# Kernel optimization log

Measured on AMD Instinct MI355X. Metric: run time of the kernel, lower is better.

## Reference

```python
import jax, jax.numpy as jnp
import numpy as np

B, C, H, W = 2, 128, 64, 64  # in_channels == mlp_dim == 128 (residual requires equality)
MLP = 128


def setup_inputs() -> dict:
    key = jax.random.key(0)
    ks = jax.random.split(key, 12)
    s = 1.0 / np.sqrt(C)
    inp = {
        "x": jax.random.normal(ks[0], (B, C, H, W), jnp.float32),
        "y": jax.random.normal(ks[1], (B, C, H, W), jnp.float32),
        # stacked params for the 4 TransLayers: [4, out, in] weights, [4, out] biases
        "Wq": jax.random.uniform(ks[2], (4, MLP, C), jnp.float32, -s, s),
        "bq": jax.random.uniform(ks[3], (4, MLP), jnp.float32, -s, s),
        "Wk": jax.random.uniform(ks[4], (4, MLP, C), jnp.float32, -s, s),
        "bk": jax.random.uniform(ks[5], (4, MLP), jnp.float32, -s, s),
        "Wv": jax.random.uniform(ks[6], (4, MLP, C), jnp.float32, -s, s),
        "bv": jax.random.uniform(ks[7], (4, MLP), jnp.float32, -s, s),
        "Wo": jax.random.uniform(ks[8], (4, MLP, C), jnp.float32, -s, s),
        "bo": jax.random.uniform(ks[9], (4, MLP), jnp.float32, -s, s),
    }
    return inp


def _conv1x1_relu(x, w, b):
    # x: [B,C,H,W], w: [O,C], b: [O]  -> [B,O,H,W]
    return jax.nn.relu(jnp.einsum('bchw,oc->bohw', x, w) + b[None, :, None, None])


def _trans_layer(x, y, wq, bq, wk, bk, wv, bv, wo, bo):
    Q = _conv1x1_relu(x, wq, bq)  # [B,C,H,W]
    K = _conv1x1_relu(y, wk, bk)
    V = _conv1x1_relu(y, wv, bv)
    b, c, h, w = Q.shape
    n = h * w
    Qf = Q.reshape(b, c, n).transpose(0, 2, 1)  # [B,N,C]
    Kf = K.reshape(b, c, n)                      # [B,C,N]
    Vf = V.reshape(b, c, n).transpose(0, 2, 1)   # [B,N,C]
    attn = jax.nn.softmax(jnp.einsum('bnc,bcm->bnm', Qf, Kf), axis=-1)  # unscaled, [B,N,N]
    wV = jnp.einsum('bnm,bmc->bnc', attn, Vf)    # [B,N,C]
    wV = wV.transpose(0, 2, 1).reshape(b, c, h, w)
    return _conv1x1_relu(wV, wo, bo) + x


def reference(x, y, Wq, bq, Wk, bk, Wv, bv, Wo, bo):
    layer = lambda i, a, b_: _trans_layer(a, b_, Wq[i], bq[i], Wk[i], bk[i],
                                          Wv[i], bv[i], Wo[i], bo[i])
    fuse_xy = layer(0, x, y)
    fuse_yz = layer(1, y, x)
    fuse_xx = layer(2, fuse_xy, fuse_xy)
    fuse_yy = layer(3, fuse_yz, fuse_yz)
    return fuse_xx + fuse_yy
```

## Files before the change

kernel.cpp:

```cpp
#include <hip/hip_runtime.h>
#include <math.h>

#define C 128
#define NSP 4096
#define LOG2E 1.4426950408889634f

typedef __attribute__((ext_vector_type(8))) short short8;
typedef __attribute__((ext_vector_type(4))) float f32x4;
typedef __attribute__((ext_vector_type(16))) float f32x16;

static __device__ __forceinline__ unsigned short f2bf(float f) {
    union { float f; unsigned u; } a; a.f = f;
    unsigned r = a.u + 0x7fffu + ((a.u >> 16) & 1u);
    return (unsigned short)(r >> 16);
}

static __device__ __forceinline__ float bf2f(unsigned short s) {
    union { unsigned u; float f; } a; a.u = (unsigned)s << 16;
    return a.f;
}

static __device__ __forceinline__ unsigned pkbf(float a, float b) {
    union { float f; unsigned u; } ua, ub; ua.f = a; ub.f = b;
    return __builtin_amdgcn_perm(ub.u + 0x8000u, ua.u + 0x8000u, 0x07060302u);
}

static __device__ __forceinline__ float ex2(float x) {
#if __has_builtin(__builtin_amdgcn_exp2f)
    return __builtin_amdgcn_exp2f(x);
#else
    return exp2f(x);
#endif
}

static __device__ __forceinline__ f32x4 mfma16(short8 a, short8 b, f32x4 c) {
    return __builtin_amdgcn_mfma_f32_16x16x32_bf16(a, b, c, 0, 0, 0);
}

static __device__ __forceinline__ f32x16 mfma32(short8 a, short8 b, f32x16 c) {
    return __builtin_amdgcn_mfma_f32_32x32x16_bf16(a, b, c, 0, 0, 0);
}

__global__ __launch_bounds__(256)
void prep_kernel(const float* __restrict__ Wq, const float* __restrict__ Wk,
                 const float* __restrict__ Wv, const float* __restrict__ Wo,
                 unsigned short* __restrict__ Wb)
{
    int gid = blockIdx.x * 256 + threadIdx.x;
    int base = gid * 8;
    int mat = base >> 14;
    int off = base & 16383;
    const float* src = (mat < 4)  ? (Wq + (size_t)mat * 16384)
                     : (mat < 8)  ? (Wk + (size_t)(mat - 4) * 16384)
                     : (mat < 12) ? (Wv + (size_t)(mat - 8) * 16384)
                                  : (Wo + (size_t)(mat - 12) * 16384);
    float scale = (mat < 4) ? LOG2E : 1.0f;
    float4 v0 = *reinterpret_cast<const float4*>(src + off);
    float4 v1 = *reinterpret_cast<const float4*>(src + off + 4);
    uint4 u;
    u.x = pkbf(v0.x * scale, v0.y * scale);
    u.y = pkbf(v0.z * scale, v0.w * scale);
    u.z = pkbf(v1.x * scale, v1.y * scale);
    u.w = pkbf(v1.z * scale, v1.w * scale);
    *reinterpret_cast<uint4*>(Wb + base) = u;
}

static __device__ __forceinline__ void stage_wb(const unsigned short* __restrict__ Wm,
                                                unsigned short* __restrict__ Wl, int t) {
#pragma unroll
    for (int i = 0; i < 8; i++) {
        int idx = i * 256 + t;
        int o = idx >> 4, c8 = (idx & 15) << 3;
        *reinterpret_cast<uint4*>(&Wl[o * 136 + c8]) =
            *reinterpret_cast<const uint4*>(Wm + o * C + c8);
    }
}

static __device__ __forceinline__ void stage_in(const float* __restrict__ In, int n0,
                                                unsigned short* __restrict__ Il, int t) {
#pragma unroll
    for (int i = 0; i < 8; i++) {
        int idx = i * 256 + t;
        int c = idx >> 4, n4 = (idx & 15) << 2;
        float4 v = *reinterpret_cast<const float4*>(In + (size_t)c * NSP + n0 + n4);
        Il[(n4 + 0) * 136 + c] = f2bf(v.x);
        Il[(n4 + 1) * 136 + c] = f2bf(v.y);
        Il[(n4 + 2) * 136 + c] = f2bf(v.z);
        Il[(n4 + 3) * 136 + c] = f2bf(v.w);
    }
}

static __device__ __forceinline__ void stage_sum32(const unsigned short* __restrict__ Op,
                                                   const float* __restrict__ Lp,
                                                   int jb, int nks, int n0,
                                                   unsigned short* __restrict__ Il, int t) {
#pragma unroll
    for (int i = 0; i < 2; i++) {
        int idx = i * 256 + t;
        int n = idx >> 4, c8 = (idx & 15) << 3;
        float o[8];
#pragma unroll
        for (int j = 0; j < 8; j++) o[j] = 0.0f;
        float Ls = 0.0f;
        for (int k = 0; k < nks; k++) {
            size_t kjb = (size_t)(k * 4 + jb);
            Ls += Lp[kjb * NSP + n0 + n];
            union { uint4 v; unsigned short s[8]; } u;
            u.v = *reinterpret_cast<const uint4*>(Op + (kjb * NSP + n0 + n) * C + c8);
#pragma unroll
            for (int j = 0; j < 8; j++) o[j] += bf2f(u.s[j]);
        }
        float inv = 1.0f / Ls;
        union { uint4 v; unsigned u[4]; } w;
        w.u[0] = pkbf(o[0] * inv, o[1] * inv);
        w.u[1] = pkbf(o[2] * inv, o[3] * inv);
        w.u[2] = pkbf(o[4] * inv, o[5] * inv);
        w.u[3] = pkbf(o[6] * inv, o[7] * inv);
        *reinterpret_cast<uint4*>(&Il[n * 136 + c8]) = w.v;
    }
}

__global__ __launch_bounds__(256)
void qkv_kernel(const float* __restrict__ qs0, const float* __restrict__ qs1,
                const float* __restrict__ kv0, const float* __restrict__ kv1,
                const unsigned short* __restrict__ Wb,
                const float* __restrict__ bq, const float* __restrict__ bk,
                const float* __restrict__ bv,
                int layer_base,
                unsigned short* __restrict__ Qb, unsigned short* __restrict__ Kb,
                unsigned short* __restrict__ Vb)
{
    __shared__ __align__(16) unsigned short Wl[128 * 136];
    __shared__ __align__(16) unsigned short Il[64 * 136];
    const int t = threadIdx.x;
    const int ntile = blockIdx.x, kind = blockIdx.y, jb = blockIdx.z;
    const int job = jb >> 1, b = jb & 1, layer = layer_base + job;
    const float* src = (kind == 0) ? (job ? qs1 : qs0) : (job ? kv1 : kv0);
    const float* In = src + (size_t)b * C * NSP;
    const unsigned short* Wm = Wb + (size_t)(kind * 4 + layer) * 16384;
    const float* bias = ((kind == 0) ? bq : (kind == 1) ? bk : bv) + layer * C;
    unsigned short* Out = ((kind == 0) ? Qb : (kind == 1) ? Kb : Vb) + (size_t)jb * NSP * C;
    const float scale = (kind == 0) ? LOG2E : 1.0f;
    const int n0 = ntile * 64;

    stage_wb(Wm, Wl, t);
    stage_in(In, n0, Il, t);
    __syncthreads();

    const int lane = t & 63, w = t >> 6, l15 = lane & 15, quad = lane >> 4;

    if (kind <= 1) {
        f32x4 acc[4][2];
#pragma unroll
        for (int nt = 0; nt < 4; nt++)
#pragma unroll
            for (int ot = 0; ot < 2; ot++)
#pragma unroll
                for (int r = 0; r < 4; r++) acc[nt][ot][r] = 0.0f;
#pragma unroll
        for (int ks = 0; ks < 4; ks++) {
            int co = ks * 32 + quad * 8;
            short8 b0 = *reinterpret_cast<const short8*>(&Wl[(w * 32 + l15) * 136 + co]);
            short8 b1 = *reinterpret_cast<const short8*>(&Wl[(w * 32 + 16 + l15) * 136 + co]);
#pragma unroll
            for (int nt = 0; nt < 4; nt++) {
                short8 a = *reinterpret_cast<const short8*>(&Il[(nt * 16 + l15) * 136 + co]);
                acc[nt][0] = mfma16(a, b0, acc[nt][0]);
                acc[nt][1] = mfma16(a, b1, acc[nt][1]);
            }
        }
        float bz0 = bias[w * 32 + l15] * scale;
        float bz1 = bias[w * 32 + 16 + l15] * scale;
#pragma unroll
        for (int nt = 0; nt < 4; nt++)
#pragma unroll
            for (int ot = 0; ot < 2; ot++)
#pragma unroll
                for (int r = 0; r < 4; r++) {
                    float v = fmaxf(acc[nt][ot][r] + (ot ? bz1 : bz0), 0.0f);
                    int n = n0 + nt * 16 + quad * 4 + r;
                    int o = w * 32 + ot * 16 + l15;
                    Out[(size_t)n * C + o] = f2bf(v);
                }
    } else {
        f32x4 acc[2][4];
#pragma unroll
        for (int ot = 0; ot < 2; ot++)
#pragma unroll
            for (int nt = 0; nt < 4; nt++)
#pragma unroll
                for (int r = 0; r < 4; r++) acc[ot][nt][r] = 0.0f;
#pragma unroll
        for (int ks = 0; ks < 4; ks++) {
            int co = ks * 32 + quad * 8;
            short8 a0 = *reinterpret_cast<const short8*>(&Wl[(w * 32 + l15) * 136 + co]);
            short8 a1 = *reinterpret_cast<const short8*>(&Wl[(w * 32 + 16 + l15) * 136 + co]);
#pragma unroll
            for (int nt = 0; nt < 4; nt++) {
                short8 bb = *reinterpret_cast<const short8*>(&Il[(nt * 16 + l15) * 136 + co]);
                acc[0][nt] = mfma16(a0, bb, acc[0][nt]);
                acc[1][nt] = mfma16(a1, bb, acc[1][nt]);
            }
        }
#pragma unroll
        for (int ot = 0; ot < 2; ot++)
#pragma unroll
            for (int r = 0; r < 4; r++) {
                int o = w * 32 + ot * 16 + quad * 4 + r;
                float bz = bias[o];
#pragma unroll
                for (int nt = 0; nt < 4; nt++) {
                    float v = fmaxf(acc[ot][nt][r] + bz, 0.0f);
                    Out[(size_t)o * NSP + n0 + nt * 16 + l15] = f2bf(v);
                }
            }
    }
}

__global__ __launch_bounds__(512)
void attn_kernel(const unsigned short* __restrict__ Qb, const unsigned short* __restrict__ Kb,
                 const unsigned short* __restrict__ Vb, unsigned short* __restrict__ Op,
                 float* __restrict__ Lp, int iters)
{
    __shared__ __align__(16) unsigned short Kl[2][32 * 136];
    __shared__ __align__(16) unsigned short Vl[2][128 * 40];
    const int t = threadIdx.x, lane = t & 63;
    const int l31 = lane & 31, hi = lane >> 5;

    const int ksz = gridDim.z;
    const int nwg = gridDim.x * gridDim.y * ksz;
    const int linear = blockIdx.x + gridDim.x * (blockIdx.y + gridDim.y * blockIdx.z);
    const int cpx = nwg >> 3;
    const int wid = (linear & 7) * cpx + (linear >> 3);
    const int ntile = wid & 15;
    const int r2 = wid >> 4;
    const int jb = r2 / ksz, kc = r2 % ksz;

    const int n0 = ntile * 256 + (t >> 6) * 32;
    const int m_begin = kc * iters * 32;
    const unsigned short* Q = Qb + (size_t)jb * NSP * C;
    const unsigned short* K = Kb + (size_t)jb * NSP * C;
    const unsigned short* V = Vb + (size_t)jb * NSP * C;

    short8 qf[8];
#pragma unroll
    for (int ks = 0; ks < 8; ks++)
        qf[ks] = *reinterpret_cast<const short8*>(
            Q + (size_t)(n0 + l31) * C + ks * 16 + hi * 8);

    f32x16 o_acc[4];
#pragma unroll
    for (int ct = 0; ct < 4; ct++)
#pragma unroll
        for (int r = 0; r < 16; r++) o_acc[ct][r] = 0.0f;
    float L = 0.0f;

    uint4 kreg, vreg;
    const int km_ = t >> 4, kc8_ = (t & 15) << 3;
    const int vc_ = t >> 2, vm8_ = (t & 3) << 3;

#define ATT_LOAD(BLK)                                                                  \
    {                                                                                  \
        int mb_ = m_begin + (BLK) * 32;                                                \
        kreg = *reinterpret_cast<const uint4*>(K + (size_t)(mb_ + km_) * C + kc8_);    \
        vreg = *reinterpret_cast<const uint4*>(V + (size_t)vc_ * NSP + mb_ + vm8_);    \
    }

#define ATT_STORE(BUF)                                                                 \
    {                                                                                  \
        *reinterpret_cast<uint4*>(&Kl[BUF][km_ * 136 + kc8_]) = kreg;                  \
        *reinterpret_cast<uint4*>(&Vl[BUF][vc_ * 40 + vm8_]) = vreg;                   \
    }

    ATT_LOAD(0);
    ATT_STORE(0);
    if (iters > 1) ATT_LOAD(1);
    __syncthreads();

    int cur = 0;
    for (int blk = 0; blk < iters; blk++) {
        const unsigned short* Kc = &Kl[cur][0];
        const unsigned short* Vc = &Vl[cur][0];

        f32x16 s;
#pragma unroll
        for (int r = 0; r < 16; r++) s[r] = 0.0f;
        __builtin_amdgcn_s_setprio(1);
#pragma unroll
        for (int ks = 0; ks < 8; ks++) {
            short8 ka = *reinterpret_cast<const short8*>(&Kc[l31 * 136 + ks * 16 + hi * 8]);
            s = mfma32(ka, qf[ks], s);
        }
        __builtin_amdgcn_s_setprio(0);

        if (blk + 1 < iters) {
            ATT_STORE(cur ^ 1);
            if (blk + 2 < iters) ATT_LOAD(blk + 2);
        }

        float ls = 0.0f;
#pragma unroll
        for (int r = 0; r < 16; r++) {
            s[r] = ex2(s[r]);
            ls += s[r];
        }
        L += ls;

        unsigned a0 = pkbf(s[0], s[1]),  a1 = pkbf(s[2], s[3]);
        unsigned b0 = pkbf(s[4], s[5]),  b1 = pkbf(s[6], s[7]);
        unsigned c0 = pkbf(s[8], s[9]),  c1 = pkbf(s[10], s[11]);
        unsigned d0 = pkbf(s[12], s[13]), d1 = pkbf(s[14], s[15]);
        asm("v_permlane32_swap_b32 %0, %1" : "+v"(a0), "+v"(b0));
        asm("v_permlane32_swap_b32 %0, %1" : "+v"(a1), "+v"(b1));
        asm("v_permlane32_swap_b32 %0, %1" : "+v"(c0), "+v"(d0));
        asm("v_permlane32_swap_b32 %0, %1" : "+v"(c1), "+v"(d1));
        union { uint4 u; short8 s8; } f0u, f1u;
        f0u.u = make_uint4(a0, a1, b0, b1);
        f1u.u = make_uint4(c0, c1, d0, d1);

        __builtin_amdgcn_s_setprio(1);
#pragma unroll
        for (int ct = 0; ct < 4; ct++) {
            short8 v0 = *reinterpret_cast<const short8*>(&Vc[(ct * 32 + l31) * 40 + hi * 8]);
            short8 v1 = *reinterpret_cast<const short8*>(&Vc[(ct * 32 + l31) * 40 + 16 + hi * 8]);
            o_acc[ct] = mfma32(v0, f0u.s8, o_acc[ct]);
            o_acc[ct] = mfma32(v1, f1u.s8, o_acc[ct]);
        }
        __builtin_amdgcn_s_setprio(0);

        __syncthreads();
        cur ^= 1;
    }

#undef ATT_LOAD
#undef ATT_STORE

    const size_t kjb = (size_t)(kc * 4 + jb);
    float Lv = L + __shfl_xor(L, 32);
    if (lane < 32) Lp[kjb * NSP + n0 + l31] = Lv;

    unsigned short* Ob = Op + kjb * NSP * C;
    const int n = n0 + l31;
    unsigned short* On = Ob + (size_t)n * C + hi * 4;
#pragma unroll
    for (int ct = 0; ct < 4; ct++)
#pragma unroll
        for (int rb = 0; rb < 4; rb++) {
            int r0 = rb * 4;
            uint2 u;
            u.x = pkbf(o_acc[ct][r0 + 0], o_acc[ct][r0 + 1]);
            u.y = pkbf(o_acc[ct][r0 + 2], o_acc[ct][r0 + 3]);
            *reinterpret_cast<uint2*>(On + ct * 32 + rb * 8) = u;
        }
}

__global__ __launch_bounds__(256)
void proj_kernel(const unsigned short* __restrict__ Op, const float* __restrict__ Lp, int nks,
                 const unsigned short* __restrict__ Wb,
                 const float* __restrict__ bo, int layer_base,
                 const float* __restrict__ res0, const float* __restrict__ res1,
                 float* __restrict__ out0, float* __restrict__ out1)
{
    __shared__ __align__(16) unsigned short Wl[128 * 136];
    __shared__ __align__(16) unsigned short Il[32 * 136];
    const int t = threadIdx.x;
    const int ntile = blockIdx.x, jb = blockIdx.y;
    const int job = jb >> 1, b = jb & 1, layer = layer_base + job;
    const float* bias = bo + layer * C;
    const float* res = (job ? res1 : res0) + (size_t)b * C * NSP;
    float* out = (job ? out1 : out0) + (size_t)b * C * NSP;
    const int n0 = ntile * 32;

    stage_wb(Wb + (size_t)(12 + layer) * 16384, Wl, t);
    stage_sum32(Op, Lp, jb, nks, n0, Il, t);
    __syncthreads();

    const int lane = t & 63, w = t >> 6, l15 = lane & 15, quad = lane >> 4;
    f32x4 acc[2][2];
#pragma unroll
    for (int ot = 0; ot < 2; ot++)
#pragma unroll
        for (int nt = 0; nt < 2; nt++)
#pragma unroll
            for (int r = 0; r < 4; r++) acc[ot][nt][r] = 0.0f;
#pragma unroll
    for (int ks = 0; ks < 4; ks++) {
        int co = ks * 32 + quad * 8;
        short8 a0 = *reinterpret_cast<const short8*>(&Wl[(w * 32 + l15) * 136 + co]);
        short8 a1 = *reinterpret_cast<const short8*>(&Wl[(w * 32 + 16 + l15) * 136 + co]);
#pragma unroll
        for (int nt = 0; nt < 2; nt++) {
            short8 bb = *reinterpret_cast<const short8*>(&Il[(nt * 16 + l15) * 136 + co]);
            acc[0][nt] = mfma16(a0, bb, acc[0][nt]);
            acc[1][nt] = mfma16(a1, bb, acc[1][nt]);
        }
    }
#pragma unroll
    for (int ot = 0; ot < 2; ot++)
#pragma unroll
        for (int r = 0; r < 4; r++) {
            int o = w * 32 + ot * 16 + quad * 4 + r;
            float bz = bias[o];
#pragma unroll
            for (int nt = 0; nt < 2; nt++) {
                int n = n0 + nt * 16 + l15;
                float v = fmaxf(acc[ot][nt][r] + bz, 0.0f) + res[(size_t)o * NSP + n];
                out[(size_t)o * NSP + n] = v;
            }
        }
}

__global__ __launch_bounds__(256)
void final_kernel(const unsigned short* __restrict__ Op, const float* __restrict__ Lp, int nks,
                  const unsigned short* __restrict__ Wb,
                  const float* __restrict__ bo,
                  const float* __restrict__ fuse0, const float* __restrict__ fuse1,
                  float* __restrict__ out)
{
    __shared__ __align__(16) unsigned short Wl[128 * 136];
    __shared__ __align__(16) unsigned short Il[32 * 136];
    const int t = threadIdx.x;
    const int ntile = blockIdx.x, b = blockIdx.y;
    const int n0 = ntile * 32;
    const int lane = t & 63, w = t >> 6, l15 = lane & 15, quad = lane >> 4;

    float tot[2][2][4];
#pragma unroll
    for (int ot = 0; ot < 2; ot++)
#pragma unroll
        for (int nt = 0; nt < 2; nt++)
#pragma unroll
            for (int r = 0; r < 4; r++) tot[ot][nt][r] = 0.0f;

    for (int j = 0; j < 2; j++) {
        if (j) __syncthreads();
        int layer = 2 + j;
        stage_wb(Wb + (size_t)(12 + layer) * 16384, Wl, t);
        stage_sum32(Op, Lp, j * 2 + b, nks, n0, Il, t);
        __syncthreads();

        f32x4 acc[2][2];
#pragma unroll
        for (int ot = 0; ot < 2; ot++)
#pragma unroll
            for (int nt = 0; nt < 2; nt++)
#pragma unroll
                for (int r = 0; r < 4; r++) acc[ot][nt][r] = 0.0f;
#pragma unroll
        for (int ks = 0; ks < 4; ks++) {
            int co = ks * 32 + quad * 8;
            short8 a0 = *reinterpret_cast<const short8*>(&Wl[(w * 32 + l15) * 136 + co]);
            short8 a1 = *reinterpret_cast<const short8*>(&Wl[(w * 32 + 16 + l15) * 136 + co]);
#pragma unroll
            for (int nt = 0; nt < 2; nt++) {
                short8 bb = *reinterpret_cast<const short8*>(&Il[(nt * 16 + l15) * 136 + co]);
                acc[0][nt] = mfma16(a0, bb, acc[0][nt]);
                acc[1][nt] = mfma16(a1, bb, acc[1][nt]);
            }
        }
        const float* bias = bo + layer * C;
        const float* fuse = (j ? fuse1 : fuse0) + (size_t)b * C * NSP;
#pragma unroll
        for (int ot = 0; ot < 2; ot++)
#pragma unroll
            for (int r = 0; r < 4; r++) {
                int o = w * 32 + ot * 16 + quad * 4 + r;
                float bz = bias[o];
#pragma unroll
                for (int nt = 0; nt < 2; nt++) {
                    int n = n0 + nt * 16 + l15;
                    tot[ot][nt][r] += fmaxf(acc[ot][nt][r] + bz, 0.0f) + fuse[(size_t)o * NSP + n];
                }
            }
    }
#pragma unroll
    for (int ot = 0; ot < 2; ot++)
#pragma unroll
        for (int r = 0; r < 4; r++) {
            int o = w * 32 + ot * 16 + quad * 4 + r;
#pragma unroll
            for (int nt = 0; nt < 2; nt++) {
                int n = n0 + nt * 16 + l15;
                out[(size_t)b * C * NSP + (size_t)o * NSP + n] = tot[ot][nt][r];
            }
        }
}

extern "C" void kernel_launch(void* const* d_in, const int* in_sizes, int n_in,
                              void* d_out, int out_size, void* d_ws, size_t ws_size,
                              hipStream_t stream)
{
    (void)in_sizes; (void)n_in; (void)out_size;
    const float* x  = (const float*)d_in[0];
    const float* y  = (const float*)d_in[1];
    const float* Wq = (const float*)d_in[2];
    const float* bq = (const float*)d_in[3];
    const float* Wk = (const float*)d_in[4];
    const float* bk = (const float*)d_in[5];
    const float* Wv = (const float*)d_in[6];
    const float* bv = (const float*)d_in[7];
    const float* Wo = (const float*)d_in[8];
    const float* bo = (const float*)d_in[9];
    float* out = (float*)d_out;
    char* ws = (char*)d_ws;

    int ks = (ws_size >= 38010880u) ? 4 : 2;
    int iters = 128 / ks;

    unsigned short* Qb = (unsigned short*)(ws);
    unsigned short* Kb = (unsigned short*)(ws + (4u << 20));
    unsigned short* Vb = (unsigned short*)(ws + (8u << 20));
    unsigned short* Op = (unsigned short*)(ws + (12u << 20));
    size_t op_bytes = (size_t)ks * 4 * NSP * C * 2;
    float* Lp = (float*)(ws + (12u << 20) + op_bytes);
    float* fuse0 = Lp + (size_t)ks * 4 * NSP;
    float* fuse1 = fuse0 + (size_t)2 * C * NSP;
    unsigned short* Wb = (unsigned short*)(fuse1 + (size_t)2 * C * NSP);

    prep_kernel<<<dim3(128), 256, 0, stream>>>(Wq, Wk, Wv, Wo, Wb);

    qkv_kernel<<<dim3(64, 3, 4), 256, 0, stream>>>(x, y, y, x, Wb, bq, bk, bv, 0,
                                                   Qb, Kb, Vb);
    attn_kernel<<<dim3(16, 4, ks), 512, 0, stream>>>(Qb, Kb, Vb, Op, Lp, iters);
    proj_kernel<<<dim3(128, 4), 256, 0, stream>>>(Op, Lp, ks, Wb, bo, 0, x, y, fuse0, fuse1);

    qkv_kernel<<<dim3(64, 3, 4), 256, 0, stream>>>(fuse0, fuse1, fuse0, fuse1, Wb,
                                                   bq, bk, bv, 2, Qb, Kb, Vb);
    attn_kernel<<<dim3(16, 4, ks), 512, 0, stream>>>(Qb, Kb, Vb, Op, Lp, iters);
    final_kernel<<<dim3(128, 2), 256, 0, stream>>>(Op, Lp, ks, Wb, bo, fuse0, fuse1, out);
}
```

Baseline: 186.4 us.

## Double attention K/V block size to halve barriers; coalesce input staging loads

```diff
diff --git a/kernel.cpp b/kernel.cpp
--- a/kernel.cpp
+++ b/kernel.cpp
@@ -79,14 +79,19 @@
 static __device__ __forceinline__ void stage_in(const float* __restrict__ In, int n0,
                                                 unsigned short* __restrict__ Il, int t) {
 #pragma unroll
-    for (int i = 0; i < 8; i++) {
+    for (int i = 0; i < 4; i++) {
         int idx = i * 256 + t;
-        int c = idx >> 4, n4 = (idx & 15) << 2;
-        float4 v = *reinterpret_cast<const float4*>(In + (size_t)c * NSP + n0 + n4);
-        Il[(n4 + 0) * 136 + c] = f2bf(v.x);
-        Il[(n4 + 1) * 136 + c] = f2bf(v.y);
-        Il[(n4 + 2) * 136 + c] = f2bf(v.z);
-        Il[(n4 + 3) * 136 + c] = f2bf(v.w);
+        int n = idx & 63, cb = idx >> 6;
+        float v[8];
+#pragma unroll
+        for (int j = 0; j < 8; j++)
+            v[j] = In[(size_t)(cb * 8 + j) * NSP + n0 + n];
+        uint4 u;
+        u.x = pkbf(v[0], v[1]);
+        u.y = pkbf(v[2], v[3]);
+        u.z = pkbf(v[4], v[5]);
+        u.w = pkbf(v[6], v[7]);
+        *reinterpret_cast<uint4*>(&Il[n * 136 + cb * 8]) = u;
     }
 }
 
@@ -222,8 +227,8 @@
                  const unsigned short* __restrict__ Vb, unsigned short* __restrict__ Op,
                  float* __restrict__ Lp, int iters)
 {
-    __shared__ __align__(16) unsigned short Kl[2][32 * 136];
-    __shared__ __align__(16) unsigned short Vl[2][128 * 40];
+    __shared__ __align__(16) unsigned short Kl[2][64 * 136];
+    __shared__ __align__(16) unsigned short Vl[2][128 * 72];
     const int t = threadIdx.x, lane = t & 63;
     const int l31 = lane & 31, hi = lane >> 5;
 
@@ -237,7 +242,7 @@
     const int jb = r2 / ksz, kc = r2 % ksz;
 
     const int n0 = ntile * 256 + (t >> 6) * 32;
-    const int m_begin = kc * iters * 32;
+    const int m_begin = kc * iters * 64;
     const unsigned short* Q = Qb + (size_t)jb * NSP * C;
     const unsigned short* K = Kb + (size_t)jb * NSP * C;
     const unsigned short* V = Vb + (size_t)jb * NSP * C;
@@ -255,21 +260,29 @@
         for (int r = 0; r < 16; r++) o_acc[ct][r] = 0.0f;
     float L = 0.0f;
 
-    uint4 kreg, vreg;
-    const int km_ = t >> 4, kc8_ = (t & 15) << 3;
-    const int vc_ = t >> 2, vm8_ = (t & 3) << 3;
-
-#define ATT_LOAD(BLK)                                                                  \
-    {                                                                                  \
-        int mb_ = m_begin + (BLK) * 32;                                                \
-        kreg = *reinterpret_cast<const uint4*>(K + (size_t)(mb_ + km_) * C + kc8_);    \
-        vreg = *reinterpret_cast<const uint4*>(V + (size_t)vc_ * NSP + mb_ + vm8_);    \
-    }
-
-#define ATT_STORE(BUF)                                                                 \
-    {                                                                                  \
-        *reinterpret_cast<uint4*>(&Kl[BUF][km_ * 136 + kc8_]) = kreg;                  \
-        *reinterpret_cast<uint4*>(&Vl[BUF][vc_ * 40 + vm8_]) = vreg;                   \
+    uint4 kreg[2], vreg[2];
+
+#define ATT_LOAD(BLK)                                                                     \
+    {                                                                                     \
+        int mb_ = m_begin + (BLK) * 64;                                                   \
+        _Pragma("unroll") for (int i = 0; i < 2; i++) {                                   \
+            int idx = i * 512 + t;                                                        \
+            int m_ = idx >> 4, c8_ = (idx & 15) << 3;                                     \
+            kreg[i] = *reinterpret_cast<const uint4*>(K + (size_t)(mb_ + m_) * C + c8_);  \
+            int c_ = idx >> 3, m8_ = (idx & 7) << 3;                                      \
+            vreg[i] = *reinterpret_cast<const uint4*>(V + (size_t)c_ * NSP + mb_ + m8_);  \
+        }                                                                                 \
+    }
+
+#define ATT_STORE(BUF)                                                                    \
+    {                                                                                     \
+        _Pragma("unroll") for (int i = 0; i < 2; i++) {                                   \
+            int idx = i * 512 + t;                                                        \
+            int m_ = idx >> 4, c8_ = (idx & 15) << 3;                                     \
+            *reinterpret_cast<uint4*>(&Kl[BUF][m_ * 136 + c8_]) = kreg[i];                \
+            int c_ = idx >> 3, m8_ = (idx & 7) << 3;                                      \
+            *reinterpret_cast<uint4*>(&Vl[BUF][c_ * 72 + m8_]) = vreg[i];                 \
+        }                                                                                 \
     }
 
     ATT_LOAD(0);
@@ -282,51 +295,57 @@
         const unsigned short* Kc = &Kl[cur][0];
         const unsigned short* Vc = &Vl[cur][0];
 
-        f32x16 s;
-#pragma unroll
-        for (int r = 0; r < 16; r++) s[r] = 0.0f;
-        __builtin_amdgcn_s_setprio(1);
-#pragma unroll
-        for (int ks = 0; ks < 8; ks++) {
-            short8 ka = *reinterpret_cast<const short8*>(&Kc[l31 * 136 + ks * 16 + hi * 8]);
-            s = mfma32(ka, qf[ks], s);
-        }
-        __builtin_amdgcn_s_setprio(0);
-
-        if (blk + 1 < iters) {
-            ATT_STORE(cur ^ 1);
-            if (blk + 2 < iters) ATT_LOAD(blk + 2);
-        }
-
-        float ls = 0.0f;
-#pragma unroll
-        for (int r = 0; r < 16; r++) {
-            s[r] = ex2(s[r]);
-            ls += s[r];
-        }
-        L += ls;
-
-        unsigned a0 = pkbf(s[0], s[1]),  a1 = pkbf(s[2], s[3]);
-        unsigned b0 = pkbf(s[4], s[5]),  b1 = pkbf(s[6], s[7]);
-        unsigned c0 = pkbf(s[8], s[9]),  c1 = pkbf(s[10], s[11]);
-        unsigned d0 = pkbf(s[12], s[13]), d1 = pkbf(s[14], s[15]);
-        asm("v_permlane32_swap_b32 %0, %1" : "+v"(a0), "+v"(b0));
-        asm("v_permlane32_swap_b32 %0, %1" : "+v"(a1), "+v"(b1));
-        asm("v_permlane32_swap_b32 %0, %1" : "+v"(c0), "+v"(d0));
-        asm("v_permlane32_swap_b32 %0, %1" : "+v"(c1), "+v"(d1));
-        union { uint4 u; short8 s8; } f0u, f1u;
-        f0u.u = make_uint4(a0, a1, b0, b1);
-        f1u.u = make_uint4(c0, c1, d0, d1);
-
-        __builtin_amdgcn_s_setprio(1);
-#pragma unroll
-        for (int ct = 0; ct < 4; ct++) {
-            short8 v0 = *reinterpret_cast<const short8*>(&Vc[(ct * 32 + l31) * 40 + hi * 8]);
-            short8 v1 = *reinterpret_cast<const short8*>(&Vc[(ct * 32 + l31) * 40 + 16 + hi * 8]);
-            o_acc[ct] = mfma32(v0, f0u.s8, o_acc[ct]);
-            o_acc[ct] = mfma32(v1, f1u.s8, o_acc[ct]);
-        }
-        __builtin_amdgcn_s_setprio(0);
+#pragma unroll
+        for (int h = 0; h < 2; h++) {
+            f32x16 s;
+#pragma unroll
+            for (int r = 0; r < 16; r++) s[r] = 0.0f;
+            __builtin_amdgcn_s_setprio(1);
+#pragma unroll
+            for (int ks = 0; ks < 8; ks++) {
+                short8 ka = *reinterpret_cast<const short8*>(
+                    &Kc[(h * 32 + l31) * 136 + ks * 16 + hi * 8]);
+                s = mfma32(ka, qf[ks], s);
+            }
+            __builtin_amdgcn_s_setprio(0);
+
+            if (h == 0 && blk + 1 < iters) {
+                ATT_STORE(cur ^ 1);
+                if (blk + 2 < iters) ATT_LOAD(blk + 2);
+            }
+
+            float ls = 0.0f;
+#pragma unroll
+            for (int r = 0; r < 16; r++) {
+                s[r] = ex2(s[r]);
+                ls += s[r];
+            }
+            L += ls;
+
+            unsigned a0 = pkbf(s[0], s[1]),  a1 = pkbf(s[2], s[3]);
+            unsigned b0 = pkbf(s[4], s[5]),  b1 = pkbf(s[6], s[7]);
+            unsigned c0 = pkbf(s[8], s[9]),  c1 = pkbf(s[10], s[11]);
+            unsigned d0 = pkbf(s[12], s[13]), d1 = pkbf(s[14], s[15]);
+            asm("v_permlane32_swap_b32 %0, %1" : "+v"(a0), "+v"(b0));
+            asm("v_permlane32_swap_b32 %0, %1" : "+v"(a1), "+v"(b1));
+            asm("v_permlane32_swap_b32 %0, %1" : "+v"(c0), "+v"(d0));
+            asm("v_permlane32_swap_b32 %0, %1" : "+v"(c1), "+v"(d1));
+            union { uint4 u; short8 s8; } f0u, f1u;
+            f0u.u = make_uint4(a0, a1, b0, b1);
+            f1u.u = make_uint4(c0, c1, d0, d1);
+
+            __builtin_amdgcn_s_setprio(1);
+#pragma unroll
+            for (int ct = 0; ct < 4; ct++) {
+                short8 v0 = *reinterpret_cast<const short8*>(
+                    &Vc[(ct * 32 + l31) * 72 + h * 32 + hi * 8]);
+                short8 v1 = *reinterpret_cast<const short8*>(
+                    &Vc[(ct * 32 + l31) * 72 + h * 32 + 16 + hi * 8]);
+                o_acc[ct] = mfma32(v0, f0u.s8, o_acc[ct]);
+                o_acc[ct] = mfma32(v1, f1u.s8, o_acc[ct]);
+            }
+            __builtin_amdgcn_s_setprio(0);
+        }
 
         __syncthreads();
         cur ^= 1;
@@ -505,7 +524,7 @@
     char* ws = (char*)d_ws;
 
     int ks = (ws_size >= 38010880u) ? 4 : 2;
-    int iters = 128 / ks;
+    int iters = 64 / ks;
 
     unsigned short* Qb = (unsigned short*)(ws);
     unsigned short* Kb = (unsigned short*)(ws + (4u << 20));
```

New measurement: 226.0 us. +21.2%, slower.
